# Optimization experiments

Measured on AMD Instinct MI355X. Metric: run time of the kernel, lower is better.

## Reference

```python
import jax, jax.numpy as jnp
import numpy as np

B, C, NX, NY = 8, 128, 256, 256
N = 32768

def setup_inputs() -> dict:
    key = jax.random.key(0)
    k1, k2 = jax.random.split(key)
    x = jax.random.normal(k1, (B, C, NX, NY), dtype=jnp.float32)
    coords = jax.random.uniform(k2, (B, N, 2), dtype=jnp.float32)
    return {"x": x, "coords": coords}

def reference(x, coords):
    b, c, nx, ny = x.shape
    # Match torch: scale by (dim-1), clamp to [0, dim], floor to int (nearest-lower gather).
    px = jnp.clip(coords[:, :, 1] * (nx - 1), 0, nx).astype(jnp.int32)  # (b, n)
    py = jnp.clip(coords[:, :, 0] * (ny - 1), 0, ny).astype(jnp.int32)  # (b, n)
    # Direct per-batch gather: out[b, c, n] = x[b, c, px[b,n], py[b,n]]
    flat_idx = px * ny + py                                             # (b, n)
    x_flat = x.reshape(b, c, nx * ny)                                   # (b, c, nx*ny)
    out = jnp.take_along_axis(x_flat, flat_idx[:, None, :], axis=2)     # (b, c, n)
    return out
```

## Files before the change

kernel.cpp:

```cpp
#include <hip/hip_runtime.h>

#define B_  8
#define C_  128
#define NX_ 256
#define NY_ 256
#define N_  32768
#define PLANE_ (NX_ * NY_)

typedef float f32x4 __attribute__((ext_vector_type(4)));

__device__ __forceinline__ int sample_idx(const float* __restrict__ coords, int b, int n) {
    const float2 cc = *reinterpret_cast<const float2*>(coords + ((size_t)b * N_ + n) * 2);
    const int px = (int)fminf(fmaxf(cc.y * (float)(NX_ - 1), 0.0f), (float)NX_);
    const int py = (int)fminf(fmaxf(cc.x * (float)(NY_ - 1), 0.0f), (float)NY_);
    return min(px * NY_ + py, PLANE_ - 1);
}

__global__ __launch_bounds__(256, 2) void gather_direct(const float* __restrict__ x,
                                                        const float* __restrict__ coords,
                                                        float* __restrict__ out) {
    const int bid = blockIdx.x;
    const int b   = bid & 7;
    const int cg  = (bid >> 3) & 1;
    const int nt  = bid >> 4;
    const int n0  = nt << 10;
    const int t   = threadIdx.x;

    int idx[4];
    #pragma unroll
    for (int k = 0; k < 4; ++k) idx[k] = sample_idx(coords, b, n0 + t + 256 * k);

    const float* __restrict__ xb = x + ((size_t)b * C_ + (size_t)cg * 64) * PLANE_;
    float* __restrict__ ob = out + ((size_t)b * C_ + (size_t)cg * 64) * N_ + n0;

    const float* __restrict__ pfb = xb + nt * 2048 + t * 8;

    #pragma unroll 2
    for (int c = 0; c < 64; ++c) {
        const int cpf = (c + 3 < 64) ? (c + 3) : 63;
        {
            const f32x4 p0 = *reinterpret_cast<const f32x4*>(pfb + (size_t)cpf * PLANE_);
            const f32x4 p1 = *reinterpret_cast<const f32x4*>(pfb + (size_t)cpf * PLANE_ + 4);
            asm volatile("" :: "v"(p0), "v"(p1));
        }
        const float* __restrict__ xp = xb + (size_t)c * PLANE_;
        float v[4];
        #pragma unroll
        for (int k = 0; k < 4; ++k) v[k] = xp[idx[k]];
        #pragma unroll
        for (int k = 0; k < 4; ++k)
            __builtin_nontemporal_store(v[k], ob + (size_t)c * N_ + t + 256 * k);
    }
}

extern "C" void kernel_launch(void* const* d_in, const int* in_sizes, int n_in,
                              void* d_out, int out_size, void* d_ws, size_t ws_size,
                              hipStream_t stream) {
    const float* x      = (const float*)d_in[0];
    const float* coords = (const float*)d_in[1];
    float* out          = (float*)d_out;
    gather_direct<<<B_ * 2 * (N_ / 1024), 256, 0, stream>>>(x, coords, out);
}
```

Before: 548.6 us.

## Retile gather to one sample per thread, batch eight channel loads, drop prefetch

```diff
diff --git a/kernel.cpp b/kernel.cpp
--- a/kernel.cpp
+++ b/kernel.cpp
@@ -7,8 +7,6 @@
 #define N_  32768
 #define PLANE_ (NX_ * NY_)
 
-typedef float f32x4 __attribute__((ext_vector_type(4)));
-
 __device__ __forceinline__ int sample_idx(const float* __restrict__ coords, int b, int n) {
     const float2 cc = *reinterpret_cast<const float2*>(coords + ((size_t)b * N_ + n) * 2);
     const int px = (int)fminf(fmaxf(cc.y * (float)(NX_ - 1), 0.0f), (float)NX_);
@@ -16,40 +14,31 @@
     return min(px * NY_ + py, PLANE_ - 1);
 }
 
-__global__ __launch_bounds__(256, 2) void gather_direct(const float* __restrict__ x,
-                                                        const float* __restrict__ coords,
-                                                        float* __restrict__ out) {
+__global__ __launch_bounds__(256) void gather_direct(const float* __restrict__ x,
+                                                     const float* __restrict__ coords,
+                                                     float* __restrict__ out) {
     const int bid = blockIdx.x;
     const int b   = bid & 7;
-    const int cg  = (bid >> 3) & 1;
-    const int nt  = bid >> 4;
-    const int n0  = nt << 10;
+    const int nt  = bid >> 3;
+    const int n0  = nt << 7;
     const int t   = threadIdx.x;
+    const int s   = t & 127;
+    const int ch  = (t >> 7) << 6;
 
-    int idx[4];
-    #pragma unroll
-    for (int k = 0; k < 4; ++k) idx[k] = sample_idx(coords, b, n0 + t + 256 * k);
+    const int idx = sample_idx(coords, b, n0 + s);
 
-    const float* __restrict__ xb = x + ((size_t)b * C_ + (size_t)cg * 64) * PLANE_;
-    float* __restrict__ ob = out + ((size_t)b * C_ + (size_t)cg * 64) * N_ + n0;
-
-    const float* __restrict__ pfb = xb + nt * 2048 + t * 8;
+    const float* __restrict__ xb = x + ((size_t)b * C_ + ch) * PLANE_;
+    float* __restrict__ ob = out + ((size_t)b * C_ + ch) * N_ + n0;
 
     #pragma unroll 2
-    for (int c = 0; c < 64; ++c) {
-        const int cpf = (c + 3 < 64) ? (c + 3) : 63;
-        {
-            const f32x4 p0 = *reinterpret_cast<const f32x4*>(pfb + (size_t)cpf * PLANE_);
-            const f32x4 p1 = *reinterpret_cast<const f32x4*>(pfb + (size_t)cpf * PLANE_ + 4);
-            asm volatile("" :: "v"(p0), "v"(p1));
-        }
-        const float* __restrict__ xp = xb + (size_t)c * PLANE_;
-        float v[4];
+    for (int c0 = 0; c0 < 64; c0 += 8) {
+        float v[8];
         #pragma unroll
-        for (int k = 0; k < 4; ++k) v[k] = xp[idx[k]];
+        for (int j = 0; j < 8; ++j)
+            v[j] = xb[(size_t)(c0 + j) * PLANE_ + idx];
         #pragma unroll
-        for (int k = 0; k < 4; ++k)
-            __builtin_nontemporal_store(v[k], ob + (size_t)c * N_ + t + 256 * k);
+        for (int j = 0; j < 8; ++j)
+            __builtin_nontemporal_store(v[j], ob + (size_t)(c0 + j) * N_ + s);
     }
 }
 
@@ -59,5 +48,5 @@
     const float* x      = (const float*)d_in[0];
     const float* coords = (const float*)d_in[1];
     float* out          = (float*)d_out;
-    gather_direct<<<B_ * 2 * (N_ / 1024), 256, 0, stream>>>(x, coords, out);
+    gather_direct<<<B_ * (N_ / 128), 256, 0, stream>>>(x, coords, out);
 }
```

Result: slower. 654.0 us (+19.2%).
